# Kernel tuning notes

Hardware: AMD Instinct MI355X
Metric: run time of the kernel (lower is better)

## Reference

```python
import jax, jax.numpy as jnp
import numpy as np

B, S, D, F, E = 4, 2048, 512, 2048, 8


def setup_inputs() -> dict:
    key = jax.random.key(0)
    ks = jax.random.split(key, 8)
    s1 = 1.0 / np.sqrt(D)
    s2 = 1.0 / np.sqrt(F)
    return {
        "hidden_states": jax.random.normal(ks[0], (B, S, D), jnp.float32),
        "gating_probs": jax.random.uniform(ks[1], (B, S, E), jnp.float32),
        "shared_gate_prob": jax.random.uniform(ks[2], (B, S, 1), jnp.float32),
        "W1": jax.random.normal(ks[3], (E, D, F), jnp.float32) * s1,
        "b1": jnp.zeros((E, F), jnp.float32),
        "W2": jax.random.normal(ks[4], (E, F, D), jnp.float32) * s2,
        "b2": jnp.zeros((E, D), jnp.float32),
        "Ws1": jax.random.normal(ks[5], (D, F), jnp.float32) * s1,
        "bs1": jnp.zeros((F,), jnp.float32),
        "Ws2": jax.random.normal(ks[6], (F, D), jnp.float32) * s2,
        "bs2": jnp.zeros((D,), jnp.float32),
    }


def reference(hidden_states, gating_probs, shared_gate_prob,
              W1, b1, W2, b2, Ws1, bs1, Ws2, bs2):
    # Dense evaluation of ALL experts over all tokens (faithful to the source).
    # h: [B, E, S, F]
    h = jax.nn.gelu(jnp.einsum("bsd,edf->besf", hidden_states, W1) + b1[None, :, None, :])
    # y: [B, E, S, D]
    y = jnp.einsum("besf,efd->besd", h, W2) + b2[None, :, None, :]
    # weighted_sum combine with per-token gating probs: [B, S, D]
    expert_output = jnp.einsum("besd,bse->bsd", y, gating_probs)
    # shared expert
    hs = jax.nn.gelu(hidden_states @ Ws1 + bs1)
    shared_out = hs @ Ws2 + bs2
    return (1.0 - shared_gate_prob) * expert_output + shared_gate_prob * shared_out
```

## Files before the change

kernel.cpp:

```cpp
#include <hip/hip_runtime.h>

#define Dm 512
#define Fm 2048
#define Mm 8192
#define KTOT 18432

typedef __attribute__((ext_vector_type(8))) short short8;
typedef __attribute__((ext_vector_type(4))) float f32x4;


__device__ __forceinline__ unsigned short f2bf(float f) {
  unsigned u = __builtin_bit_cast(unsigned, f);
  u = (u + 0x7FFFu + ((u >> 16) & 1u)) >> 16;
  return (unsigned short)u;
}

__device__ __forceinline__ float fast_exp2(float x) {
  float r; asm("v_exp_f32 %0, %1" : "=v"(r) : "v"(x)); return r;
}
__device__ __forceinline__ float fast_rcp(float x) {
  float r; asm("v_rcp_f32 %0, %1" : "=v"(r) : "v"(x)); return r;
}

__device__ __forceinline__ void gload_lds16(const void* g, void* lp) {
  __builtin_amdgcn_global_load_lds(
      (const __attribute__((address_space(1))) void*)(unsigned long long)(g),
      (__attribute__((address_space(3))) void*)(unsigned)(unsigned long long)(lp),
      16, 0, 0);
}

__device__ __forceinline__ f32x4 mfma16(short8 a, short8 b, f32x4 c) {
  asm("v_mfma_f32_16x16x32_bf16 %0, %1, %2, %0" : "+v"(c) : "v"(a), "v"(b));
  return c;
}


__global__ void cvtx_k(const float* __restrict__ src, unsigned short* __restrict__ dst, int n) {
  int i = (blockIdx.x * 256 + threadIdx.x) * 4;
  if (i >= n) return;
  const float4 v = *(const float4*)(src + i);
  unsigned a = (unsigned)f2bf(v.x) | ((unsigned)f2bf(v.y) << 16);
  unsigned b = (unsigned)f2bf(v.z) | ((unsigned)f2bf(v.w) << 16);
  uint2 o; o.x = a; o.y = b;
  *(uint2*)(dst + i) = o;
}

__global__ void wts_k(const float* __restrict__ gp, const float* __restrict__ sg,
                      float* __restrict__ wts) {
  int t = blockIdx.x * 256 + threadIdx.x;
  if (t >= Mm) return;
  float s = sg[t];
  float om = 1.0f - s;
#pragma unroll
  for (int e = 0; e < 8; ++e) wts[t * 9 + e] = om * gp[t * 8 + e];
  wts[t * 9 + 8] = s;
}

__global__ void wt_k(const float* __restrict__ W1, const float* __restrict__ Ws1,
                     const float* __restrict__ W2, const float* __restrict__ Ws2,
                     unsigned short* __restrict__ W1T, unsigned short* __restrict__ W2T) {
  __shared__ float tile[32][33];
  const int tx = threadIdx.x, ty = threadIdx.y;
  int bid = blockIdx.x;
  if (bid < 9216) {
    const int e = bid >> 10;
    const int rem = bid & 1023;
    const float* src = (e < 8) ? (W1 + (size_t)e * Dm * Fm) : Ws1;
    const int c0 = (rem & 63) << 5;
    const int r0 = (rem >> 6) << 5;
#pragma unroll
    for (int j = ty; j < 32; j += 8) tile[j][tx] = src[(size_t)(r0 + j) * Fm + c0 + tx];
    __syncthreads();
    unsigned short* de = W1T + (size_t)e * Fm * Dm;
#pragma unroll
    for (int j = ty; j < 32; j += 8) de[(size_t)(c0 + j) * Dm + r0 + tx] = f2bf(tile[tx][j]);
  } else {
    bid -= 9216;
    const int e = bid >> 10;
    const int rem = bid & 1023;
    const float* src = (e < 8) ? (W2 + (size_t)e * Fm * Dm) : Ws2;
    const int c0 = (rem & 15) << 5;
    const int r0 = (rem >> 4) << 5;
#pragma unroll
    for (int j = ty; j < 32; j += 8) tile[j][tx] = src[(size_t)(r0 + j) * Dm + c0 + tx];
    __syncthreads();
#pragma unroll
    for (int j = ty; j < 32; j += 8)
      W2T[(size_t)(c0 + j) * KTOT + (size_t)e * Fm + r0 + tx] = f2bf(tile[tx][j]);
  }
}


__global__ __launch_bounds__(256)
void gemm1_k(const unsigned short* __restrict__ Xb,
             const unsigned short* __restrict__ W1T,
             const float* __restrict__ b1, const float* __restrict__ bs1,
             const float* __restrict__ wts,
             unsigned short* __restrict__ Hs,
             int gbase, int Gg, int ldH) {
  __shared__ __attribute__((aligned(16))) unsigned short As[2][128 * 64];
  __shared__ __attribute__((aligned(16))) unsigned short Bs[2][128 * 64];

  const int tid = threadIdx.x, l = tid & 63, w = tid >> 6;
  const int wr = w >> 1, wc = w & 1;
  const int nwg = Gg << 10;
  const int wg = (blockIdx.x & 7) * (nwg >> 3) + (blockIdx.x >> 3);
  const int el = wg >> 10;
  const int rem = wg & 1023;
  const int grp = rem >> 7;
  const int sub = rem & 127;
  const int tn = (sub & 15) << 7;
  const int tm = ((grp << 3) + (sub >> 4)) << 7;
  const int eg = gbase + el;
  const unsigned short* BT = W1T + (size_t)eg * Fm * Dm;
  const float* bias = (eg < 8) ? (b1 + (size_t)eg * Fm) : bs1;

  f32x4 acc[4][4];
  const f32x4 zz = {0.f, 0.f, 0.f, 0.f};
#pragma unroll
  for (int mi = 0; mi < 4; ++mi)
#pragma unroll
    for (int ni = 0; ni < 4; ++ni) acc[mi][ni] = zz;

  const int srow = tid >> 3;
  const int sc = ((tid & 7) ^ (srow & 7)) << 3;

#define STAGE1(buf, ks)                                                          \
  {                                                                              \
    _Pragma("unroll")                                                            \
    for (int i = 0; i < 4; ++i) {                                                \
      const int row = i * 32 + srow;                                             \
      gload_lds16(Xb + (size_t)(tm + row) * Dm + (ks) + sc,                      \
                  (char*)As[buf] + i * 4096 + tid * 16);                         \
      gload_lds16(BT + (size_t)(tn + row) * Dm + (ks) + sc,                      \
                  (char*)Bs[buf] + i * 4096 + tid * 16);                         \
    }                                                                            \
  }

  STAGE1(0, 0);
  __syncthreads();

  for (int t = 0; t < 8; ++t) {
    const int cur = t & 1;
    if (t < 7) STAGE1(cur ^ 1, (t + 1) << 6);
#pragma unroll
    for (int kk = 0; kk < 2; ++kk) {
      const int kbx = (kk * 64 + ((l >> 4) << 4)) ^ ((l & 7) << 4);
      short8 af[4], bfr[4];
#pragma unroll
      for (int mi = 0; mi < 4; ++mi)
        af[mi] = *(const short8*)((const char*)As[cur] + ((wr * 64 + mi * 16 + (l & 15)) << 7) + kbx);
#pragma unroll
      for (int ni = 0; ni < 4; ++ni)
        bfr[ni] = *(const short8*)((const char*)Bs[cur] + ((wc * 64 + ni * 16 + (l & 15)) << 7) + kbx);
#pragma unroll
      for (int mi = 0; mi < 4; ++mi)
#pragma unroll
        for (int ni = 0; ni < 4; ++ni)
          acc[mi][ni] = mfma16(af[mi], bfr[ni], acc[mi][ni]);
    }
    if (t < 7) __syncthreads();
  }
#undef STAGE1

  const int row0 = tm + wr * 64 + ((l >> 4) << 2);
  const int col0 = tn + wc * 64 + (l & 15);
  const size_t hb = (size_t)el * Fm;
  float bv[4];
#pragma unroll
  for (int ni = 0; ni < 4; ++ni) bv[ni] = bias[col0 + ni * 16];

  const float Ac = -2.3022120f;
  const float Bc = -0.10294341f;

#pragma unroll
  for (int mi = 0; mi < 4; ++mi) {
#pragma unroll
    for (int r = 0; r < 4; ++r) {
      const int rr = row0 + mi * 16 + r;
      const float wt = wts[(size_t)rr * 9 + eg];
      float g[4];
#pragma unroll
      for (int ni = 0; ni < 4; ++ni) {
        const float v = acc[mi][ni][r] + bv[ni];
        const float t2 = v * fmaf(Bc, v * v, Ac);
        g[ni] = wt * v * fast_rcp(1.0f + fast_exp2(t2));
      }
      unsigned pk0, pk1;
      asm("v_cvt_pk_bf16_f32 %0, %1, %2" : "=v"(pk0) : "v"(g[0]), "v"(g[1]));
      asm("v_cvt_pk_bf16_f32 %0, %1, %2" : "=v"(pk1) : "v"(g[2]), "v"(g[3]));
      unsigned short* hp = Hs + (size_t)rr * ldH + hb + col0;
      hp[0]  = (unsigned short)pk0;
      hp[16] = (unsigned short)(pk0 >> 16);
      hp[32] = (unsigned short)pk1;
      hp[48] = (unsigned short)(pk1 >> 16);
    }
  }
}


__global__ __launch_bounds__(256)
void gemm2_k(const unsigned short* __restrict__ A, int lda,
             const unsigned short* __restrict__ BT, int ldb,
             float* __restrict__ out,
             const float* __restrict__ wts,
             const float* __restrict__ b2, const float* __restrict__ bs2,
             int Kt, int g0) {
  __shared__ __attribute__((aligned(16))) unsigned short As[3][128 * 64];
  __shared__ __attribute__((aligned(16))) unsigned short Bs[3][64 * 64];

  const int tid = threadIdx.x, l = tid & 63, w = tid >> 6;
  const int wr = w >> 1, wc = w & 1;
  const int wg = (blockIdx.x & 7) * 64 + (blockIdx.x >> 3);
  const int gm = wg >> 6;
  const int sub = wg & 63;
  const int tn = (sub & 7) << 6;
  const int tm = ((gm << 3) + (sub >> 3)) << 7;

  f32x4 acc[4][2];
  const f32x4 zz = {0.f, 0.f, 0.f, 0.f};
#pragma unroll
  for (int mi = 0; mi < 4; ++mi)
#pragma unroll
    for (int ni = 0; ni < 2; ++ni) acc[mi][ni] = zz;

  const int srow = tid >> 3;
  const int sc = ((tid & 7) ^ (srow & 7)) << 3;

#define STAGE2(buf, ks)                                                          \
  {                                                                              \
    _Pragma("unroll")                                                            \
    for (int i = 0; i < 4; ++i) {                                                \
      const int row = i * 32 + srow;                                             \
      gload_lds16(A + (size_t)(tm + row) * lda + (ks) + sc,                      \
                  (char*)As[buf] + i * 4096 + tid * 16);                         \
    }                                                                            \
    _Pragma("unroll")                                                            \
    for (int i = 0; i < 2; ++i) {                                                \
      const int row = i * 32 + srow;                                             \
      gload_lds16(BT + (size_t)(tn + row) * ldb + (ks) + sc,                     \
                  (char*)Bs[buf] + i * 4096 + tid * 16);                         \
    }                                                                            \
  }

  const int NT = Kt >> 6;
  STAGE2(0, 0);
  STAGE2(1, 64);

  for (int t = 0; t < NT; ++t) {
    const int cur = t % 3;
    if (t + 1 < NT) { asm volatile("s_waitcnt vmcnt(6)" ::: "memory"); }
    else            { asm volatile("s_waitcnt vmcnt(0)" ::: "memory"); }
    __builtin_amdgcn_s_barrier();
    __builtin_amdgcn_sched_barrier(0);
    if (t + 2 < NT) {
      const int nb = (t + 2) % 3;
      STAGE2(nb, (t + 2) << 6);
    }
#pragma unroll
    for (int kk = 0; kk < 2; ++kk) {
      const int kbx = (kk * 64 + ((l >> 4) << 4)) ^ ((l & 7) << 4);
      short8 af[4], bfr[2];
#pragma unroll
      for (int mi = 0; mi < 4; ++mi)
        af[mi] = *(const short8*)((const char*)As[cur] + ((wr * 64 + mi * 16 + (l & 15)) << 7) + kbx);
#pragma unroll
      for (int ni = 0; ni < 2; ++ni)
        bfr[ni] = *(const short8*)((const char*)Bs[cur] + ((wc * 32 + ni * 16 + (l & 15)) << 7) + kbx);
#pragma unroll
      for (int mi = 0; mi < 4; ++mi)
#pragma unroll
        for (int ni = 0; ni < 2; ++ni)
          acc[mi][ni] = mfma16(af[mi], bfr[ni], acc[mi][ni]);
    }
  }
#undef STAGE2

  const int row0 = tm + wr * 64 + ((l >> 4) << 2);
  const int col0 = tn + wc * 32 + (l & 15);

  if (g0) {
    float bcol[2][9];
#pragma unroll
    for (int ni = 0; ni < 2; ++ni) {
      const int c = col0 + ni * 16;
#pragma unroll
      for (int e = 0; e < 8; ++e) bcol[ni][e] = b2[(e << 9) + c];
      bcol[ni][8] = bs2[c];
    }
#pragma unroll
    for (int mi = 0; mi < 4; ++mi)
#pragma unroll
      for (int r = 0; r < 4; ++r) {
        const int rr = row0 + mi * 16 + r;
        const float* wrow = wts + (size_t)rr * 9;
#pragma unroll
        for (int ni = 0; ni < 2; ++ni) {
          float b = 0.f;
#pragma unroll
          for (int e = 0; e < 9; ++e) b += wrow[e] * bcol[ni][e];
          out[(size_t)rr * Dm + col0 + ni * 16] = acc[mi][ni][r] + b;
        }
      }
  } else {
#pragma unroll
    for (int mi = 0; mi < 4; ++mi)
#pragma unroll
      for (int r = 0; r < 4; ++r) {
        const size_t rb = (size_t)(row0 + mi * 16 + r) * Dm;
#pragma unroll
        for (int ni = 0; ni < 2; ++ni)
          out[rb + col0 + ni * 16] += acc[mi][ni][r];
      }
  }
}


extern "C" void kernel_launch(void* const* d_in, const int* in_sizes, int n_in,
                              void* d_out, int out_size, void* d_ws, size_t ws_size,
                              hipStream_t stream) {
  const float* x   = (const float*)d_in[0];
  const float* gp  = (const float*)d_in[1];
  const float* sg  = (const float*)d_in[2];
  const float* W1  = (const float*)d_in[3];
  const float* b1  = (const float*)d_in[4];
  const float* W2  = (const float*)d_in[5];
  const float* b2  = (const float*)d_in[6];
  const float* Ws1 = (const float*)d_in[7];
  const float* bs1 = (const float*)d_in[8];
  const float* Ws2 = (const float*)d_in[9];
  const float* bs2 = (const float*)d_in[10];
  float* out = (float*)d_out;

  const size_t szXb  = (size_t)Mm * Dm * 2;
  const size_t szWts = (size_t)Mm * 9 * 4;
  const size_t szW1T = (size_t)9 * Fm * Dm * 2;
  const size_t szW2T = (size_t)9 * Fm * Dm * 2;
  const size_t base  = szXb + szWts + szW1T + szW2T;

  int G;
  if      (ws_size >= base + (size_t)Mm * 9 * Fm * 2) G = 9;
  else if (ws_size >= base + (size_t)Mm * 3 * Fm * 2) G = 3;
  else if (ws_size >= base + (size_t)Mm * 2 * Fm * 2) G = 2;
  else if (ws_size >= base + (size_t)Mm * 1 * Fm * 2) G = 1;
  else return;

  char* ws = (char*)d_ws;
  unsigned short* Xb  = (unsigned short*)(ws);
  float*          wts = (float*)(ws + szXb);
  unsigned short* W1T = (unsigned short*)(ws + szXb + szWts);
  unsigned short* W2T = (unsigned short*)(ws + szXb + szWts + szW1T);
  unsigned short* Hs  = (unsigned short*)(ws + base);
  const int ldH = G * Fm;

  cvtx_k<<<dim3((Mm * Dm) / 1024), dim3(256), 0, stream>>>(x, Xb, Mm * Dm);
  wts_k<<<dim3(Mm / 256), dim3(256), 0, stream>>>(gp, sg, wts);
  wt_k<<<dim3(2 * 9 * 1024), dim3(32, 8), 0, stream>>>(W1, Ws1, W2, Ws2, W1T, W2T);

  for (int gb = 0; gb < 9; gb += G) {
    const int Gg = (9 - gb < G) ? (9 - gb) : G;
    gemm1_k<<<dim3(Gg * 1024), dim3(256), 0, stream>>>(
        Xb, W1T, b1, bs1, wts, Hs, gb, Gg, ldH);
    gemm2_k<<<dim3(512), dim3(256), 0, stream>>>(
        Hs, ldH, W2T + (size_t)gb * Fm, KTOT, out, wts, b2, bs2, Gg * Fm, gb == 0 ? 1 : 0);
  }
}
```

Baseline: 423.7 us.

## Shrink gemm1 N-tile to 64 and triple-buffer its K loop with vmcnt waits

gemm1 moves from a 128x128 output tile with double buffering to a 128x64 tile with a three-stage LDS ring, prefetching two K-steps ahead and using fused s_waitcnt vmcnt plus s_barrier instead of __syncthreads. This doubles the workgroup count and halves per-wave accumulators, which should raise occupancy and hide global-load latency better. In exchange, each block has less data reuse, so more A-tile traffic goes to L2. Both GEMM loops are also marked unroll 1 to keep code size and register use down.

Result: slower. 469.0 us (+10.7%).

```diff
diff --git a/kernel.cpp b/kernel.cpp
--- a/kernel.cpp
+++ b/kernel.cpp
@@ -33,6 +33,8 @@
   asm("v_mfma_f32_16x16x32_bf16 %0, %1, %2, %0" : "+v"(c) : "v"(a), "v"(b));
   return c;
 }
+
+#define WAIT_BARRIER(n) asm volatile("s_waitcnt vmcnt(" #n ")\n\ts_barrier" ::: "memory")
 
 
 __global__ void cvtx_k(const float* __restrict__ src, unsigned short* __restrict__ dst, int n) {
@@ -98,29 +100,29 @@
              const float* __restrict__ wts,
              unsigned short* __restrict__ Hs,
              int gbase, int Gg, int ldH) {
-  __shared__ __attribute__((aligned(16))) unsigned short As[2][128 * 64];
-  __shared__ __attribute__((aligned(16))) unsigned short Bs[2][128 * 64];
+  __shared__ __attribute__((aligned(16))) unsigned short As[3][128 * 64];
+  __shared__ __attribute__((aligned(16))) unsigned short Bs[3][64 * 64];
 
   const int tid = threadIdx.x, l = tid & 63, w = tid >> 6;
   const int wr = w >> 1, wc = w & 1;
-  const int nwg = Gg << 10;
+  const int nwg = Gg << 11;
   const int wg = (blockIdx.x & 7) * (nwg >> 3) + (blockIdx.x >> 3);
-  const int el = wg >> 10;
-  const int rem = wg & 1023;
-  const int grp = rem >> 7;
-  const int sub = rem & 127;
-  const int tn = (sub & 15) << 7;
-  const int tm = ((grp << 3) + (sub >> 4)) << 7;
+  const int el = wg >> 11;
+  const int rem = wg & 2047;
+  const int grp = rem >> 8;
+  const int sub = rem & 255;
+  const int tn = (sub & 31) << 6;
+  const int tm = ((grp << 3) + (sub >> 5)) << 7;
   const int eg = gbase + el;
   const unsigned short* BT = W1T + (size_t)eg * Fm * Dm;
   const float* bias = (eg < 8) ? (b1 + (size_t)eg * Fm) : bs1;
 
-  f32x4 acc[4][4];
+  f32x4 acc[4][2];
   const f32x4 zz = {0.f, 0.f, 0.f, 0.f};
 #pragma unroll
   for (int mi = 0; mi < 4; ++mi)
 #pragma unroll
-    for (int ni = 0; ni < 4; ++ni) acc[mi][ni] = zz;
+    for (int ni = 0; ni < 2; ++ni) acc[mi][ni] = zz;
 
   const int srow = tid >> 3;
   const int sc = ((tid & 7) ^ (srow & 7)) << 3;
@@ -132,43 +134,53 @@
       const int row = i * 32 + srow;                                             \
       gload_lds16(Xb + (size_t)(tm + row) * Dm + (ks) + sc,                      \
                   (char*)As[buf] + i * 4096 + tid * 16);                         \
+    }                                                                            \
+    _Pragma("unroll")                                                            \
+    for (int i = 0; i < 2; ++i) {                                                \
+      const int row = i * 32 + srow;                                             \
       gload_lds16(BT + (size_t)(tn + row) * Dm + (ks) + sc,                      \
                   (char*)Bs[buf] + i * 4096 + tid * 16);                         \
     }                                                                            \
   }
 
   STAGE1(0, 0);
-  __syncthreads();
-
+  STAGE1(1, 64);
+
+#pragma unroll 1
   for (int t = 0; t < 8; ++t) {
-    const int cur = t & 1;
-    if (t < 7) STAGE1(cur ^ 1, (t + 1) << 6);
+    const int cur = t % 3;
+    if (t + 1 < 8) { WAIT_BARRIER(6); }
+    else           { WAIT_BARRIER(0); }
+    __builtin_amdgcn_sched_barrier(0);
+    if (t + 2 < 8) {
+      const int nb = (t + 2) % 3;
+      STAGE1(nb, (t + 2) << 6);
+    }
 #pragma unroll
     for (int kk = 0; kk < 2; ++kk) {
       const int kbx = (kk * 64 + ((l >> 4) << 4)) ^ ((l & 7) << 4);
-      short8 af[4], bfr[4];
+      short8 af[4], bfr[2];
 #pragma unroll
       for (int mi = 0; mi < 4; ++mi)
         af[mi] = *(const short8*)((const char*)As[cur] + ((wr * 64 + mi * 16 + (l & 15)) << 7) + kbx);
 #pragma unroll
-      for (int ni = 0; ni < 4; ++ni)
-        bfr[ni] = *(const short8*)((const char*)Bs[cur] + ((wc * 64 + ni * 16 + (l & 15)) << 7) + kbx);
+      for (int ni = 0; ni < 2; ++ni)
+        bfr[ni] = *(const short8*)((const char*)Bs[cur] + ((wc * 32 + ni * 16 + (l & 15)) << 7) + kbx);
 #pragma unroll
       for (int mi = 0; mi < 4; ++mi)
 #pragma unroll
-        for (int ni = 0; ni < 4; ++ni)
+        for (int ni = 0; ni < 2; ++ni)
           acc[mi][ni] = mfma16(af[mi], bfr[ni], acc[mi][ni]);
     }
-    if (t < 7) __syncthreads();
   }
 #undef STAGE1
 
   const int row0 = tm + wr * 64 + ((l >> 4) << 2);
-  const int col0 = tn + wc * 64 + (l & 15);
+  const int col0 = tn + wc * 32 + (l & 15);
   const size_t hb = (size_t)el * Fm;
-  float bv[4];
-#pragma unroll
-  for (int ni = 0; ni < 4; ++ni) bv[ni] = bias[col0 + ni * 16];
+  float bv[2];
+#pragma unroll
+  for (int ni = 0; ni < 2; ++ni) bv[ni] = bias[col0 + ni * 16];
 
   const float Ac = -2.3022120f;
   const float Bc = -0.10294341f;
@@ -179,21 +191,18 @@
     for (int r = 0; r < 4; ++r) {
       const int rr = row0 + mi * 16 + r;
       const float wt = wts[(size_t)rr * 9 + eg];
-      float g[4];
-#pragma unroll
-      for (int ni = 0; ni < 4; ++ni) {
+      float g[2];
+#pragma unroll
+      for (int ni = 0; ni < 2; ++ni) {
         const float v = acc[mi][ni][r] + bv[ni];
         const float t2 = v * fmaf(Bc, v * v, Ac);
         g[ni] = wt * v * fast_rcp(1.0f + fast_exp2(t2));
       }
-      unsigned pk0, pk1;
+      unsigned pk0;
       asm("v_cvt_pk_bf16_f32 %0, %1, %2" : "=v"(pk0) : "v"(g[0]), "v"(g[1]));
-      asm("v_cvt_pk_bf16_f32 %0, %1, %2" : "=v"(pk1) : "v"(g[2]), "v"(g[3]));
       unsigned short* hp = Hs + (size_t)rr * ldH + hb + col0;
       hp[0]  = (unsigned short)pk0;
       hp[16] = (unsigned short)(pk0 >> 16);
-      hp[32] = (unsigned short)pk1;
-      hp[48] = (unsigned short)(pk1 >> 16);
     }
   }
 }
@@ -247,11 +256,11 @@
   STAGE2(0, 0);
   STAGE2(1, 64);
 
+#pragma unroll 1
   for (int t = 0; t < NT; ++t) {
     const int cur = t % 3;
-    if (t + 1 < NT) { asm volatile("s_waitcnt vmcnt(6)" ::: "memory"); }
-    else            { asm volatile("s_waitcnt vmcnt(0)" ::: "memory"); }
-    __builtin_amdgcn_s_barrier();
+    if (t + 1 < NT) { WAIT_BARRIER(6); }
+    else            { WAIT_BARRIER(0); }
     __builtin_amdgcn_sched_barrier(0);
     if (t + 2 < NT) {
       const int nb = (t + 2) % 3;
@@ -359,7 +368,7 @@
 
   for (int gb = 0; gb < 9; gb += G) {
     const int Gg = (9 - gb < G) ? (9 - gb) : G;
-    gemm1_k<<<dim3(Gg * 1024), dim3(256), 0, stream>>>(
+    gemm1_k<<<dim3(Gg * 2048), dim3(256), 0, stream>>>(
         Xb, W1T, b1, bs1, wts, Hs, gb, Gg, ldH);
     gemm2_k<<<dim3(512), dim3(256), 0, stream>>>(
         Hs, ldH, W2T + (size_t)gb * Fm, KTOT, out, wts, b2, bs2, Gg * Fm, gb == 0 ? 1 : 0);
```
